# Kernel optimization log

Hardware: AMD Instinct MI355X
Metric: run time of the kernel (lower is better)

## Reference

```python
import jax, jax.numpy as jnp
import numpy as np
import math

DN = ('NCHW', 'OIHW', 'NCHW')

def conv(x, w, b, stride=1, pad=0):
    y = jax.lax.conv_general_dilated(x, w, (stride, stride), ((pad, pad), (pad, pad)), dimension_numbers=DN)
    return y + b[None, :, None, None]

def conv_t(x, w, b, stride=2, k=4, p=1):
    # torch ConvTranspose2d: weight (Cin, Cout, kH, kW). Equivalent fractionally-strided conv:
    w2 = jnp.transpose(w[:, :, ::-1, ::-1], (1, 0, 2, 3))  # -> (Cout, Cin, kH, kW), spatially flipped
    pp = k - 1 - p
    y = jax.lax.conv_general_dilated(x, w2, (1, 1), ((pp, pp), (pp, pp)), lhs_dilation=(stride, stride), dimension_numbers=DN)
    return y + b[None, :, None, None]

def res_stack(h, w1, b1, w2, b2):
    # w1: [L, rh, nh, 3, 3], w2: [L, nh, rh, 1, 1]
    for i in range(w1.shape[0]):
        t = conv(jax.nn.relu(h), w1[i], b1[i], 1, 1)
        t = conv(jax.nn.relu(t), w2[i], b2[i], 1, 0)
        h = h + t
    return jax.nn.relu(h)

def setup_inputs() -> dict:
    key = jax.random.key(0)
    ks = jax.random.split(key, 16)
    D, K = 64, 512
    limit = math.sqrt(3.0 / D)
    def w(k, shape, scale=0.05):
        return (jax.random.normal(k, shape, dtype=jnp.float32) * scale)
    return {
        'x': jax.random.normal(ks[0], (16, 3, 256, 256), dtype=jnp.float32),
        'enc_w0': w(ks[1], (64, 3, 4, 4)), 'enc_b0': jnp.zeros((64,), jnp.float32),
        'enc_w1': w(ks[2], (128, 64, 4, 4)), 'enc_b1': jnp.zeros((128,), jnp.float32),
        'enc_wf': w(ks[3], (128, 128, 3, 3)), 'enc_bf': jnp.zeros((128,), jnp.float32),
        'enc_res_w1': w(ks[4], (2, 32, 128, 3, 3)), 'enc_res_b1': jnp.zeros((2, 32), jnp.float32),
        'enc_res_w2': w(ks[5], (2, 128, 32, 1, 1)), 'enc_res_b2': jnp.zeros((2, 128), jnp.float32),
        'pre_w': w(ks[6], (64, 128, 1, 1)), 'pre_b': jnp.zeros((64,), jnp.float32),
        'codebook': jax.random.uniform(ks[7], (D, K), jnp.float32, -limit, limit),
        'dec_w': w(ks[8], (128, 64, 3, 3)), 'dec_b': jnp.zeros((128,), jnp.float32),
        'dec_res_w1': w(ks[9], (2, 32, 128, 3, 3)), 'dec_res_b1': jnp.zeros((2, 32), jnp.float32),
        'dec_res_w2': w(ks[10], (2, 128, 32, 1, 1)), 'dec_res_b2': jnp.zeros((2, 128), jnp.float32),
        'up_w0': w(ks[11], (128, 64, 4, 4)), 'up_b0': jnp.zeros((64,), jnp.float32),
        'up_w1': w(ks[12], (64, 3, 4, 4)), 'up_b1': jnp.zeros((3,), jnp.float32),
    }

def reference(x, enc_w0, enc_b0, enc_w1, enc_b1, enc_wf, enc_bf,
              enc_res_w1, enc_res_b1, enc_res_w2, enc_res_b2,
              pre_w, pre_b, codebook,
              dec_w, dec_b, dec_res_w1, dec_res_b1, dec_res_w2, dec_res_b2,
              up_w0, up_b0, up_w1, up_b1):
    # --- Encoder ---
    h = jax.nn.relu(conv(x, enc_w0, enc_b0, 2, 1))
    h = jax.nn.relu(conv(h, enc_w1, enc_b1, 2, 1))
    h = conv(h, enc_wf, enc_bf, 1, 1)
    h = res_stack(h, enc_res_w1, enc_res_b1, enc_res_w2, enc_res_b2)
    z = conv(h, pre_w, pre_b, 1, 0)  # [B, 64, 64, 64]
    # --- Vector quantizer (cdist + argmin + gather, straight-through) ---
    B, D, H, W = z.shape
    flat = jnp.transpose(z, (0, 2, 3, 1)).reshape(-1, D)  # [BHW, D]
    dist = (flat ** 2).sum(1, keepdims=True) - 2.0 * (flat @ codebook) + (codebook ** 2).sum(0)[None, :]
    idx = jnp.argmin(dist, axis=1)  # [BHW]
    q = codebook.T[idx].reshape(B, H, W, D).transpose(0, 3, 1, 2)
    zq = z + jax.lax.stop_gradient(q - z)  # straight-through estimator
    # --- Decoder ---
    h = conv(zq, dec_w, dec_b, 1, 1)
    h = res_stack(h, dec_res_w1, dec_res_b1, dec_res_w2, dec_res_b2)
    h = jax.nn.relu(conv_t(h, up_w0, up_b0, 2, 4, 1))
    x_recon = conv_t(h, up_w1, up_b1, 2, 4, 1)
    return x_recon
```

## Files before the change

### kernel.cpp

```cpp
#include <hip/hip_runtime.h>
#include <math.h>


#define DEV __device__ __forceinline__

DEV int rfl(int v) { return __builtin_amdgcn_readfirstlane(v); }

DEV void async_copy16(const float* g, float* l) {
  __builtin_amdgcn_global_load_lds(
      (const __attribute__((address_space(1))) void*)g,
      (__attribute__((address_space(3))) void*)l, 16, 0, 0);
}

typedef __attribute__((ext_vector_type(8))) _Float16 h16x8;
typedef __attribute__((ext_vector_type(4))) float f32x4;

DEV ushort f2h(float f) {
  _Float16 h = (_Float16)f;
  return __builtin_bit_cast(ushort, h);
}
DEV float h2f(ushort u) { return (float)__builtin_bit_cast(_Float16, u); }
DEV uint pk(ushort a, ushort b) { return (uint)a | ((uint)b << 16); }

template<int CIN, int COT>
__global__ __launch_bounds__(256) void prep_w3s(
    const float* __restrict__ w, ushort* __restrict__ wpk) {
  constexpr int nCh = CIN / 32, nM = COT / 16;
  const int t = blockIdx.x * 256 + threadIdx.x;
  if (t >= 9 * nCh * nM * 64) return;
  const int l = t & 63;
  const int m = (t >> 6) % nM;
  const int sid = t / (64 * nM);
  const int ch = sid / 9, khkw = sid % 9;
  const int co = m * 16 + (l & 15);
  const int k8 = (l >> 4) * 8;
  const int sw = (16 * l) ^ ((l & 4) ? 8 : 0);
  ushort* slab = wpk + (size_t)sid * (nM * 1024) + m * 1024;
#pragma unroll
  for (int i = 0; i < 8; i++) {
    const int ci = ch * 32 + k8 + i;
    const float v = w[((size_t)co * CIN + ci) * 9 + khkw];
    const ushort hi = f2h(v);
    slab[sw + i]       = hi;
    slab[(sw ^ 8) + i] = f2h((v - h2f(hi)) * 2048.0f);
  }
}

template<int CIN, int COT>
__global__ __launch_bounds__(256) void prep_w4s(
    const float* __restrict__ w, ushort* __restrict__ wpk) {
  const int t = blockIdx.x * 256 + threadIdx.x;
  if (t >= 16384) return;
  const int l = t & 63;
  const int m = (t >> 6) & 7;
  const int sid = t >> 9;
  const int step = sid >> 3, rr = (sid >> 2) & 1, kw = sid & 3;
  const int ch = step >> 1, h = step & 1;
  const int kh = 2 * h + rr;
  const int tap = kh * 4 + kw;
  const int co = m * 16 + (l & 15);
  const int k8 = (l >> 4) * 8;
  const int sw = (16 * l) ^ ((l & 4) ? 8 : 0);
  ushort* slab = wpk + (size_t)sid * 8192 + m * 1024;
#pragma unroll
  for (int i = 0; i < 8; i++) {
    const int ci = ch * 32 + k8 + i;
    const float v = w[((size_t)co * CIN + ci) * 16 + tap];
    const ushort hi = f2h(v);
    slab[sw + i]       = hi;
    slab[(sw ^ 8) + i] = f2h((v - h2f(hi)) * 2048.0f);
  }
}

template<int CIN, int COT>
__global__ __launch_bounds__(256) void prep_wts(
    const float* __restrict__ w, ushort* __restrict__ wpk) {
  constexpr int nCh = CIN / 32, nM = COT / 16;
  const int t = blockIdx.x * 256 + threadIdx.x;
  if (t >= 16 * nCh * nM * 64) return;
  const int l = t & 63;
  const int m = (t >> 6) % nM;
  const int sid = t / (64 * nM);
  const int ch = sid >> 4, idx = sid & 15;
  const int ord[16] = {15, 13, 14, 12, 7, 11, 5, 6, 9, 10, 4, 8, 3, 1, 2, 0};
  const int tap = ord[idx];
  const int kh = tap >> 2, kw = tap & 3;
  const int co = m * 16 + (l & 15);
  const int k8 = (l >> 4) * 8;
  const int sw = (16 * l) ^ ((l & 4) ? 8 : 0);
  ushort* slab = wpk + (size_t)sid * (nM * 1024) + m * 1024;
#pragma unroll
  for (int i = 0; i < 8; i++) {
    const int ci = ch * 32 + k8 + i;
    const float v = w[(((size_t)ci * COT + co) * 4 + kh) * 4 + kw];
    const ushort hi = f2h(v);
    slab[sw + i]       = hi;
    slab[(sw ^ 8) + i] = f2h((v - h2f(hi)) * 2048.0f);
  }
}

__global__ __launch_bounds__(256) void prep_cb(
    const float* __restrict__ cb, ushort* __restrict__ cbpk) {
  const int t = blockIdx.x * 256 + threadIdx.x;
  const int l = t & 63;
  const int m = (t >> 6) & 31;
  const int c = t >> 11;
  const int entry = m * 16 + (l & 15);
  ushort* o = cbpk + (size_t)t * 16;
#pragma unroll
  for (int i = 0; i < 8; i++) {
    const int d = c * 32 + (l >> 4) * 8 + i;
    const float v = cb[d * 512 + entry];
    const ushort hi = f2h(v);
    o[i]     = hi;
    o[8 + i] = f2h((v - h2f(hi)) * 2048.0f);
  }
}

__global__ __launch_bounds__(256) void cvt_cbn(
    const float* __restrict__ cb, float* __restrict__ cbn) {
  const int k = blockIdx.x * 256 + threadIdx.x;
  if (k >= 512) return;
  double s = 0.0;
  for (int d = 0; d < 64; d++) {
    const double c = (double)cb[d * 512 + k];
    s = fma(c, c, s);
  }
  cbn[k] = (float)s;
}

__global__ __launch_bounds__(256) void vq_mfma(
    const float* __restrict__ cb, const ushort* __restrict__ cbpk,
    const float* __restrict__ cbn, float* __restrict__ zq) {
  const int tid = threadIdx.x;
  const int l = tid & 63;
  const int w = rfl(tid >> 6);
  const int n = blockIdx.x >> 6, row = blockIdx.x & 63;
  float* zp = zq + (size_t)n * 262144 + row * 64;
  const int pos = w * 16 + (l & 15);

  h16x8 zh[2], zl[2];
#pragma unroll
  for (int c = 0; c < 2; c++) {
#pragma unroll
    for (int i = 0; i < 8; i++) {
      const int d = c * 32 + (l >> 4) * 8 + i;
      const float v = zp[(size_t)d * 4096 + pos];
      const _Float16 h = (_Float16)v;
      zh[c][i] = h;
      zl[c][i] = (_Float16)((v - (float)h) * 2048.0f);
    }
  }

  const float SCL = 1.0f / 2048.0f;
  float bestd = 1e30f;
  int best = 0;
  for (int grp = 0; grp < 4; grp++) {
    f32x4 aH[8], aM[8];
#pragma unroll
    for (int m = 0; m < 8; m++) {
      aH[m] = (f32x4){0.f, 0.f, 0.f, 0.f};
      aM[m] = (f32x4){0.f, 0.f, 0.f, 0.f};
    }
#pragma unroll
    for (int c = 0; c < 2; c++) {
#pragma unroll
      for (int m = 0; m < 8; m++) {
        const ushort* ap = cbpk + ((size_t)(c * 32 + grp * 8 + m) * 64 + l) * 16;
        const h16x8 ah = *(const h16x8*)ap;
        const h16x8 al = *(const h16x8*)(ap + 8);
        aH[m] = __builtin_amdgcn_mfma_f32_16x16x32_f16(ah, zh[c], aH[m], 0, 0, 0);
        aM[m] = __builtin_amdgcn_mfma_f32_16x16x32_f16(al, zh[c], aM[m], 0, 0, 0);
        aM[m] = __builtin_amdgcn_mfma_f32_16x16x32_f16(ah, zl[c], aM[m], 0, 0, 0);
      }
    }
#pragma unroll
    for (int m = 0; m < 8; m++) {
#pragma unroll
      for (int j = 0; j < 4; j++) {
        const int k = grp * 128 + m * 16 + ((l >> 4) << 2) + j;
        const float dd = aH[m][j] + aM[m][j] * SCL;
        const float dist = fmaf(-2.0f, dd, cbn[k]);
        if (dist < bestd) { bestd = dist; best = k; }
      }
    }
  }

#pragma unroll
  for (int off = 16; off <= 32; off <<= 1) {
    const float d2 = __shfl_xor(bestd, off, 64);
    const int i2 = __shfl_xor(best, off, 64);
    if (d2 < bestd || (d2 == bestd && i2 < best)) { bestd = d2; best = i2; }
  }

#pragma unroll
  for (int i = 0; i < 16; i++) {
    const int d = (l >> 4) * 16 + i;
    zp[(size_t)d * 4096 + pos] = cb[d * 512 + best];
  }
}

template<int CIN, int COT, bool RELU_OUT>
__global__ __launch_bounds__(256, 2) void conv4s2_mfma(
    const float* __restrict__ x, const ushort* __restrict__ wpk,
    const float* __restrict__ bias, float* __restrict__ y) {
  constexpr int nCh = CIN / 32, nM = COT / 16;
  constexpr int nStep = nCh * 2;
  constexpr int nTap = nStep * 8;
  __shared__ ushort act[2][2][2][66][40];
  __shared__ ushort wlds[2][8192];
  const int tid = threadIdx.x;
  const int l = tid & 63;
  const int wv = rfl(tid >> 6);
  const int ho = (blockIdx.x & 7) * 8 + (blockIdx.x >> 3);
  const int n = blockIdx.z;

  {
    uint* lp = (uint*)&act[0][0][0][0][0];
    for (int s = tid; s < 16 * 20; s += 256) {
      const int c = s / 20, w32 = s % 20;
      const int which = c & 1, rest = c >> 1;
      lp[(size_t)(rest * 66 + (which ? 65 : 0)) * 20 + w32] = 0;
    }
  }

  const float* xn = x + ((size_t)n * CIN) * 16384;

  float2 sreg[2][4][2];
  float rmask[2];
  auto LOADG = [&](int step) {
    const int ch = step >> 1, h = step & 1;
#pragma unroll
    for (int rr = 0; rr < 2; rr++) {
      const int ir = 2 * ho - 1 + 2 * h + rr;
      const bool ok = (ir >= 0) && (ir < 128);
      const int irc = ok ? ir : 0;
      rmask[rr] = ok ? 1.0f : 0.0f;
#pragma unroll
      for (int cc = 0; cc < 4; cc++) {
        const int ci0 = ch * 32 + cc * 8 + wv * 2;
        sreg[rr][cc][0] = *(const float2*)(xn + (size_t)ci0 * 16384 + irc * 128 + 2 * l);
        sreg[rr][cc][1] = *(const float2*)(xn + (size_t)(ci0 + 1) * 16384 + irc * 128 + 2 * l);
      }
    }
  };
  auto WRITE = [&]() {
    uint* base = (uint*)&act[0][0][0][0][0];
#pragma unroll
    for (int rr = 0; rr < 2; rr++) {
#pragma unroll
      for (int cc = 0; cc < 4; cc++) {
        const float e0 = sreg[rr][cc][0].x * rmask[rr], o0 = sreg[rr][cc][0].y * rmask[rr];
        const float e1 = sreg[rr][cc][1].x * rmask[rr], o1 = sreg[rr][cc][1].y * rmask[rr];
        const ushort he0 = f2h(e0), ho_0 = f2h(o0);
        const ushort he1 = f2h(e1), ho_1 = f2h(o1);
        const ushort le0 = f2h((e0 - h2f(he0)) * 2048.0f);
        const ushort lo0 = f2h((o0 - h2f(ho_0)) * 2048.0f);
        const ushort le1 = f2h((e1 - h2f(he1)) * 2048.0f);
        const ushort lo1 = f2h((o1 - h2f(ho_1)) * 2048.0f);
        const int u = cc * 4 + wv;
        const size_t sl20 = (size_t)(l + 1) * 20 + u;
        base[(size_t)((0 * 2 + rr) * 2 + 0) * 1320 + sl20] = pk(he0, he1);
        base[(size_t)((0 * 2 + rr) * 2 + 1) * 1320 + sl20] = pk(ho_0, ho_1);
        base[(size_t)((1 * 2 + rr) * 2 + 0) * 1320 + sl20] = pk(le0, le1);
        base[(size_t)((1 * 2 + rr) * 2 + 1) * 1320 + sl20] = pk(lo0, lo1);
      }
    }
  };
  auto STAGEW = [&](int t, int buf) {
    const ushort* src = wpk + (size_t)t * 8192;
    ushort* dst = &wlds[buf][0];
#pragma unroll
    for (int j = 0; j < 4; j++)
      async_copy16((const float*)(src + (j * 256 + tid) * 8),
                   (float*)(dst + (j * 256 + tid) * 8));
  };

  f32x4 accH[nM], accM[nM];
#pragma unroll
  for (int m = 0; m < nM; m++) {
    const int co = m * 16 + ((l >> 4) << 2);
    accH[m] = (f32x4){bias[co], bias[co + 1], bias[co + 2], bias[co + 3]};
    accM[m] = (f32x4){0.f, 0.f, 0.f, 0.f};
  }

  const int pb = wv * 16;
  const int sw = (16 * l) ^ ((l & 4) ? 8 : 0);
  STAGEW(0, 0);
  LOADG(0);
  int tcnt = 0;
  for (int step = 0; step < nStep; step++) {
    __syncthreads();
    WRITE();
    __syncthreads();
#pragma unroll
    for (int rr = 0; rr < 2; rr++) {
#pragma unroll
      for (int kw = 0; kw < 4; kw++) {
        if (!(rr == 0 && kw == 0)) __syncthreads();
        if (tcnt + 1 < nTap) STAGEW(tcnt + 1, (tcnt + 1) & 1);
        if (rr == 0 && kw == 0 && step + 1 < nStep) LOADG(step + 1);
        const ushort* wb = &wlds[tcnt & 1][0];
        const int eo = (kw == 0 || kw == 2) ? 1 : 0;
        const int sh = (kw == 0) ? 0 : (kw == 3) ? 2 : 1;
        const int sl = pb + (l & 15) + sh;
        const h16x8 bh = *(const h16x8*)(&act[0][rr][eo][sl][(l >> 4) * 8]);
        const h16x8 bl = *(const h16x8*)(&act[1][rr][eo][sl][(l >> 4) * 8]);
#pragma unroll
        for (int m = 0; m < nM; m++) {
          const h16x8 ah = *(const h16x8*)(wb + m * 1024 + sw);
          const h16x8 al = *(const h16x8*)(wb + m * 1024 + (sw ^ 8));
          accH[m] = __builtin_amdgcn_mfma_f32_16x16x32_f16(ah, bh, accH[m], 0, 0, 0);
          accM[m] = __builtin_amdgcn_mfma_f32_16x16x32_f16(al, bh, accM[m], 0, 0, 0);
          accM[m] = __builtin_amdgcn_mfma_f32_16x16x32_f16(ah, bl, accM[m], 0, 0, 0);
        }
        tcnt++;
      }
    }
  }

  const float SCL = 1.0f / 2048.0f;
  const int pos = pb + (l & 15);
  const int r4 = (l >> 4) << 2;
#pragma unroll
  for (int m = 0; m < nM; m++) {
    const int co = m * 16 + r4;
    float* yp = y + (((size_t)(n * COT + co)) * 64 + ho) * 64 + pos;
#pragma unroll
    for (int j = 0; j < 4; j++) {
      float v = accH[m][j] + accM[m][j] * SCL;
      if (RELU_OUT) v = fmaxf(v, 0.f);
      yp[(size_t)j * 4096] = v;
    }
  }
}

template<int CIN, int COT, int TILE, bool RELU_IN>
__global__ __launch_bounds__(256, 2) void conv3_mfma2(
    const float* __restrict__ x, const ushort* __restrict__ wpk,
    const float* __restrict__ bias, float* __restrict__ y) {
  constexpr int nCh = CIN / 32, nMf = COT / 16, nMt = TILE / 16;
  constexpr int nTap = nCh * 9;
  __shared__ ushort act[2][4 * 66 * 40];
  __shared__ ushort wlds[2][nMt * 1024];
  const int tid = threadIdx.x;
  const int l = tid & 63;
  const int wv = rfl(tid >> 6);
  const int r0 = blockIdx.x * 2;
  const int hblk = blockIdx.y;
  const int n = blockIdx.z;

  {
    uint* lp = (uint*)&act[0][0];
    for (int s = tid; s < 16 * 20; s += 256) {
      const int c = s / 20, w32 = s % 20;
      const int which = c & 1;
      const int rowrel = (c >> 1) & 3;
      const int plane  = c >> 3;
      lp[(size_t)(plane * 264 + rowrel * 66 + (which ? 65 : 0)) * 20 + w32] = 0;
    }
  }

  const float* xn = x + ((size_t)n * CIN) * 4096;

  float sreg[4][4][2];
  auto LOADG = [&](int ch) {
#pragma unroll
    for (int rr = 0; rr < 4; rr++) {
      const int ir = r0 - 1 + rr;
      const bool ok = (ir >= 0) && (ir < 64);
#pragma unroll
      for (int cc = 0; cc < 4; cc++) {
        const int ci0 = ch * 32 + cc * 8 + wv * 2;
        sreg[rr][cc][0] = ok ? xn[((size_t)ci0 * 64 + ir) * 64 + l] : 0.f;
        sreg[rr][cc][1] = ok ? xn[((size_t)(ci0 + 1) * 64 + ir) * 64 + l] : 0.f;
      }
    }
  };
  auto WRITE = [&]() {
    uint* ph = (uint*)&act[0][0];
    uint* pl = (uint*)&act[1][0];
#pragma unroll
    for (int rr = 0; rr < 4; rr++) {
#pragma unroll
      for (int cc = 0; cc < 4; cc++) {
        float v0 = sreg[rr][cc][0], v1 = sreg[rr][cc][1];
        if (RELU_IN) { v0 = fmaxf(v0, 0.f); v1 = fmaxf(v1, 0.f); }
        const ushort h0 = f2h(v0), h1 = f2h(v1);
        const ushort m0 = f2h((v0 - h2f(h0)) * 2048.0f);
        const ushort m1 = f2h((v1 - h2f(h1)) * 2048.0f);
        const int idx = (rr * 66 + (l + 1)) * 20 + cc * 4 + wv;
        ph[idx] = (uint)h0 | ((uint)h1 << 16);
        pl[idx] = (uint)m0 | ((uint)m1 << 16);
      }
    }
  };
  auto STAGEW = [&](int t, int buf) {
    const ushort* src = wpk + (size_t)t * (nMf * 1024) + hblk * (nMt * 1024);
    ushort* dst = &wlds[buf][0];
#pragma unroll
    for (int j = 0; j < nMt / 2; j++)
      async_copy16((const float*)(src + (j * 256 + tid) * 8),
                   (float*)(dst + (j * 256 + tid) * 8));
  };

  f32x4 accH[2][nMt], accM[2][nMt];
#pragma unroll
  for (int m = 0; m < nMt; m++) {
    const int co = hblk * TILE + m * 16 + ((l >> 4) << 2);
    const f32x4 b4 = (f32x4){bias[co], bias[co + 1], bias[co + 2], bias[co + 3]};
#pragma unroll
    for (int ro = 0; ro < 2; ro++) {
      accH[ro][m] = b4;
      accM[ro][m] = (f32x4){0.f, 0.f, 0.f, 0.f};
    }
  }

  const int pb = wv * 16;
  const int sw = (16 * l) ^ ((l & 4) ? 8 : 0);
  STAGEW(0, 0);
  LOADG(0);
  int tcnt = 0;
  for (int ch = 0; ch < nCh; ch++) {
    __syncthreads();
    WRITE();
    __syncthreads();
#pragma unroll
    for (int kh = 0; kh < 3; kh++) {
#pragma unroll
      for (int kw = 0; kw < 3; kw++) {
        if (!(kh == 0 && kw == 0)) __syncthreads();
        if (tcnt + 1 < nTap) STAGEW(tcnt + 1, (tcnt + 1) & 1);
        if (kh == 0 && kw == 0 && ch + 1 < nCh) LOADG(ch + 1);
        const ushort* wb = &wlds[tcnt & 1][0];
        h16x8 bh[2], bl[2];
#pragma unroll
        for (int ro = 0; ro < 2; ro++) {
          const int slot = (ro + kh) * 66 + pb + (l & 15) + kw;
          bh[ro] = *(const h16x8*)(&act[0][0] + slot * 40 + (l >> 4) * 8);
          bl[ro] = *(const h16x8*)(&act[1][0] + slot * 40 + (l >> 4) * 8);
        }
#pragma unroll
        for (int m = 0; m < nMt; m++) {
          const h16x8 ah = *(const h16x8*)(wb + m * 1024 + sw);
          const h16x8 al = *(const h16x8*)(wb + m * 1024 + (sw ^ 8));
#pragma unroll
          for (int ro = 0; ro < 2; ro++) {
            accH[ro][m] = __builtin_amdgcn_mfma_f32_16x16x32_f16(ah, bh[ro], accH[ro][m], 0, 0, 0);
            accM[ro][m] = __builtin_amdgcn_mfma_f32_16x16x32_f16(al, bh[ro], accM[ro][m], 0, 0, 0);
            accM[ro][m] = __builtin_amdgcn_mfma_f32_16x16x32_f16(ah, bl[ro], accM[ro][m], 0, 0, 0);
          }
        }
        tcnt++;
      }
    }
  }

  const float SCL = 1.0f / 2048.0f;
  const int pos = pb + (l & 15);
  const int r4 = (l >> 4) << 2;
#pragma unroll
  for (int ro = 0; ro < 2; ro++) {
#pragma unroll
    for (int m = 0; m < nMt; m++) {
      const int co = hblk * TILE + m * 16 + r4;
      float* yp = y + (((size_t)(n * COT + co)) * 64 + (r0 + ro)) * 64 + pos;
#pragma unroll
      for (int j = 0; j < 4; j++)
        yp[(size_t)j * 4096] = accH[ro][m][j] + accM[ro][m][j] * SCL;
    }
  }
}

template<int CIN, int COT, bool RELU_OUT>
__global__ __launch_bounds__(256, 2) void convt_mfma(
    const float* __restrict__ x, const ushort* __restrict__ wpk,
    const float* __restrict__ bias, float* __restrict__ y) {
  constexpr int nCh = CIN / 32, nM = COT / 16;
  constexpr int nPair = nCh * 8;
  __shared__ ushort act[2][3 * 66 * 40];
  __shared__ ushort wlds[2][2 * nM * 1024];
  const int tid = threadIdx.x;
  const int l = tid & 63;
  const int wv = rfl(tid >> 6);
  const int a = blockIdx.x;
  const int n = blockIdx.z;

  {
    uint* lp = (uint*)&act[0][0];
    for (int s = tid; s < 12 * 20; s += 256) {
      const int c = s / 20, w32 = s % 20;
      const int which = c & 1;
      const int rowrel = (c >> 1) % 3;
      const int plane  = (c >> 1) / 3;
      lp[(size_t)(plane * 198 + rowrel * 66 + (which ? 65 : 0)) * 20 + w32] = 0;
    }
  }

  const float* xn = x + ((size_t)n * CIN) * 4096;

  float sreg[3][4][2];
  auto LOADG = [&](int ch) {
#pragma unroll
    for (int rr = 0; rr < 3; rr++) {
      const int ir = a - 1 + rr;
      const bool ok = (ir >= 0) && (ir < 64);
#pragma unroll
      for (int cc = 0; cc < 4; cc++) {
        const int ci0 = ch * 32 + cc * 8 + wv * 2;
        sreg[rr][cc][0] = ok ? xn[((size_t)ci0 * 64 + ir) * 64 + l] : 0.f;
        sreg[rr][cc][1] = ok ? xn[((size_t)(ci0 + 1) * 64 + ir) * 64 + l] : 0.f;
      }
    }
  };
  auto WRITE = [&]() {
    uint* ph = (uint*)&act[0][0];
    uint* pl = (uint*)&act[1][0];
#pragma unroll
    for (int rr = 0; rr < 3; rr++) {
#pragma unroll
      for (int cc = 0; cc < 4; cc++) {
        const float v0 = sreg[rr][cc][0], v1 = sreg[rr][cc][1];
        const ushort h0 = f2h(v0), h1 = f2h(v1);
        const ushort m0 = f2h((v0 - h2f(h0)) * 2048.0f);
        const ushort m1 = f2h((v1 - h2f(h1)) * 2048.0f);
        const int idx = (rr * 66 + (l + 1)) * 20 + cc * 4 + wv;
        ph[idx] = (uint)h0 | ((uint)h1 << 16);
        pl[idx] = (uint)m0 | ((uint)m1 << 16);
      }
    }
  };
  auto STAGEW2 = [&](int p, int buf) {
    const ushort* src = wpk + (size_t)p * (2 * nM * 1024);
    ushort* dst = &wlds[buf][0];
#pragma unroll
    for (int j = 0; j < nM; j++)
      async_copy16((const float*)(src + (j * 256 + tid) * 8),
                   (float*)(dst + (j * 256 + tid) * 8));
  };

  f32x4 aH[4][nM], aM[4][nM];
#pragma unroll
  for (int m = 0; m < nM; m++) {
    const int co = m * 16 + ((l >> 4) << 2);
    const f32x4 b4 = (f32x4){bias[co], bias[co + 1], bias[co + 2], bias[co + 3]};
#pragma unroll
    for (int o = 0; o < 4; o++) { aH[o][m] = b4; aM[o][m] = (f32x4){0.f,0.f,0.f,0.f}; }
  }

  const int pb = wv * 16;
  const int sw = (16 * l) ^ ((l & 4) ? 8 : 0);
  STAGEW2(0, 0);
  LOADG(0);
  int pcnt = 0;

#define CT_TAP(WOFS, RR, DD, OIDX) {                                          \
    const int slot = (RR) * 66 + pb + (l & 15) + 1 + (DD);                    \
    const h16x8 bh = *(const h16x8*)(&act[0][0] + slot * 40 + (l >> 4) * 8);  \
    const h16x8 bl = *(const h16x8*)(&act[1][0] + slot * 40 + (l >> 4) * 8);  \
    _Pragma("unroll")                                                         \
    for (int m = 0; m < nM; m++) {                                            \
      const h16x8 ah = *(const h16x8*)(wb + (WOFS) + m * 1024 + sw);          \
      const h16x8 al = *(const h16x8*)(wb + (WOFS) + m * 1024 + (sw ^ 8));    \
      aH[OIDX][m] = __builtin_amdgcn_mfma_f32_16x16x32_f16(ah, bh, aH[OIDX][m], 0, 0, 0); \
      aM[OIDX][m] = __builtin_amdgcn_mfma_f32_16x16x32_f16(al, bh, aM[OIDX][m], 0, 0, 0); \
      aM[OIDX][m] = __builtin_amdgcn_mfma_f32_16x16x32_f16(ah, bl, aM[OIDX][m], 0, 0, 0); \
    }}
#define CT_PHASE(RRA, DDA, OA, RRB, DDB, OB) {                                \
    if (!first) __syncthreads();                                              \
    first = false;                                                            \
    if (pcnt + 1 < nPair) STAGEW2(pcnt + 1, (pcnt + 1) & 1);                  \
    if (doLoad) { if (ch + 1 < nCh) LOADG(ch + 1); doLoad = false; }          \
    const ushort* wb = &wlds[pcnt & 1][0];                                    \
    CT_TAP(0, RRA, DDA, OA)                                                   \
    CT_TAP(nM * 1024, RRB, DDB, OB)                                           \
    pcnt++; }

  for (int ch = 0; ch < nCh; ch++) {
    __syncthreads();
    WRITE();
    __syncthreads();
    bool first = true, doLoad = true;
    CT_PHASE(0, -1, 0,  0,  0, 0)
    CT_PHASE(0,  0, 1,  0, +1, 1)
    CT_PHASE(1, -1, 0,  1, -1, 2)
    CT_PHASE(1,  0, 0,  1,  0, 1)
    CT_PHASE(1,  0, 2,  1,  0, 3)
    CT_PHASE(1, +1, 1,  1, +1, 3)
    CT_PHASE(2, -1, 2,  2,  0, 2)
    CT_PHASE(2,  0, 3,  2, +1, 3)
  }
#undef CT_TAP
#undef CT_PHASE

  const float SCL = 1.0f / 2048.0f;
  const int b = pb + (l & 15);
  const int oh0 = 2 * a;
  const int r4 = (l >> 4) << 2;
#pragma unroll
  for (int m = 0; m < nM; m++) {
    const int co = m * 16 + r4;
#pragma unroll
    for (int j = 0; j < 4; j++) {
      float v0e = aH[0][m][j] + aM[0][m][j] * SCL;
      float v0o = aH[1][m][j] + aM[1][m][j] * SCL;
      float v1e = aH[2][m][j] + aM[2][m][j] * SCL;
      float v1o = aH[3][m][j] + aM[3][m][j] * SCL;
      if (RELU_OUT) {
        v0e = fmaxf(v0e, 0.f); v0o = fmaxf(v0o, 0.f);
        v1e = fmaxf(v1e, 0.f); v1o = fmaxf(v1o, 0.f);
      }
      float* row0 = y + (((size_t)(n * COT + co + j)) * 128 + oh0) * 128;
      ((float2*)row0)[b] = make_float2(v0e, v0o);
      ((float2*)(row0 + 128))[b] = make_float2(v1e, v1o);
    }
  }
}

template<int CIN, int COT, bool RELU_OUT, int OW>
__global__ __launch_bounds__(256) void conv4s2_row(
    const float* __restrict__ x, const float* __restrict__ w,
    const float* __restrict__ bias, float* __restrict__ y,
    int Hout, int Cout) {
  const int Win = OW * 2, Hin = Hout * 2;
  const int t = blockIdx.x * 256 + threadIdx.x;
  const int wo = t & (OW - 1);
  const int ho = rfl(t / OW);
  const int co0 = blockIdx.y * COT, n = blockIdx.z;

  float acc[COT];
#pragma unroll
  for (int u = 0; u < COT; u++) acc[u] = bias[co0 + u];

  const int iw0 = 2 * wo - 1;
  const int cA = iw0 < 0 ? 0 : iw0;
  const bool mA = iw0 >= 0;
  const int cD = (iw0 + 3 < Win) ? iw0 + 3 : Win - 1;
  const bool mD = iw0 + 3 < Win;

  for (int ci = 0; ci < CIN; ci++) {
    const float* xp = x + ((size_t)(n * CIN + ci)) * Hin * Win;
    const float* wp = w + ((size_t)(co0 * CIN + ci)) * 16;
#pragma unroll
    for (int kh = 0; kh < 4; kh++) {
      const int ih = 2 * ho - 1 + kh;
      if (ih >= 0 && ih < Hin) {
        const float* row = xp + (size_t)ih * Win;
        float x0 = row[cA];      x0 = mA ? x0 : 0.f;
        float x1 = row[iw0 + 1];
        float x2 = row[iw0 + 2];
        float x3 = row[cD];      x3 = mD ? x3 : 0.f;
#pragma unroll
        for (int u = 0; u < COT; u++) {
          const float* wr = wp + u * CIN * 16 + kh * 4;
          acc[u] = fmaf(x0, wr[0], acc[u]);
          acc[u] = fmaf(x1, wr[1], acc[u]);
          acc[u] = fmaf(x2, wr[2], acc[u]);
          acc[u] = fmaf(x3, wr[3], acc[u]);
        }
      }
    }
  }
#pragma unroll
  for (int u = 0; u < COT; u++) {
    float v = acc[u];
    if (RELU_OUT) v = fmaxf(v, 0.f);
    y[(((size_t)(n * Cout + co0 + u)) * Hout + ho) * OW + wo] = v;
  }
}

template<int CIN, int COT, bool RELU_IN, bool ACCUM, bool RELU_OUT>
__global__ __launch_bounds__(256) void conv1x1_v4(
    const float* __restrict__ x, const float* __restrict__ w,
    const float* __restrict__ bias, float* __restrict__ y,
    int HW, int Cout) {
  const int p = (blockIdx.x * 256 + threadIdx.x) * 4;
  const int co0 = blockIdx.y * COT, n = blockIdx.z;

  float4 acc[COT];
#pragma unroll
  for (int u = 0; u < COT; u++) {
    const float b = bias[co0 + u];
    acc[u] = make_float4(b, b, b, b);
  }
  for (int ci = 0; ci < CIN; ci++) {
    float4 xv = *(const float4*)&x[((size_t)(n * CIN + ci)) * HW + p];
    if (RELU_IN) {
      xv.x = fmaxf(xv.x, 0.f); xv.y = fmaxf(xv.y, 0.f);
      xv.z = fmaxf(xv.z, 0.f); xv.w = fmaxf(xv.w, 0.f);
    }
#pragma unroll
    for (int u = 0; u < COT; u++) {
      const float wv = w[(co0 + u) * CIN + ci];
      acc[u].x = fmaf(xv.x, wv, acc[u].x);
      acc[u].y = fmaf(xv.y, wv, acc[u].y);
      acc[u].z = fmaf(xv.z, wv, acc[u].z);
      acc[u].w = fmaf(xv.w, wv, acc[u].w);
    }
  }
#pragma unroll
  for (int u = 0; u < COT; u++) {
    float4* yp = (float4*)&y[((size_t)(n * Cout + co0 + u)) * HW + p];
    float4 r = acc[u];
    if (ACCUM) {
      float4 h = *yp;
      r.x += h.x; r.y += h.y; r.z += h.z; r.w += h.w;
    }
    if (RELU_OUT) {
      r.x = fmaxf(r.x, 0.f); r.y = fmaxf(r.y, 0.f);
      r.z = fmaxf(r.z, 0.f); r.w = fmaxf(r.w, 0.f);
    }
    *yp = r;
  }
}

template<int CIN, int COT, bool RELU_IN, bool RELU_OUT, int WH>
__global__ __launch_bounds__(256) void convt_row(
    const float* __restrict__ x, const float* __restrict__ w,
    const float* __restrict__ bias, float* __restrict__ y,
    int Hin, int Cout) {
  const int Hout = Hin * 2;
  const int t = blockIdx.x * 256 + threadIdx.x;
  const int a = t & (WH - 1);
  const int oh = rfl(t / WH);
  const int co0 = blockIdx.y * COT, n = blockIdx.z;

  float acc0[COT], acc1[COT];
#pragma unroll
  for (int u = 0; u < COT; u++) { acc0[u] = bias[co0 + u]; acc1[u] = bias[co0 + u]; }

  const int cm = a > 0 ? a - 1 : 0;
  const bool mm = a > 0;
  const int cp = a < WH - 1 ? a + 1 : WH - 1;
  const bool mp = a < WH - 1;

  const int kh0 = (oh + 1) & 1;
#pragma unroll
  for (int dh = 0; dh < 2; dh++) {
    const int kh = kh0 + 2 * dh;
    const int ih = (oh + 1 - kh) >> 1;
    if (ih >= 0 && ih < Hin) {
      for (int ci = 0; ci < CIN; ci++) {
        const float* row = x + (((size_t)(n * CIN + ci)) * Hin + ih) * WH;
        float x0  = row[a];
        float xm1 = row[cm];  xm1 = mm ? xm1 : 0.f;
        float xp1 = row[cp];  xp1 = mp ? xp1 : 0.f;
        if (RELU_IN) {
          x0 = fmaxf(x0, 0.f); xm1 = fmaxf(xm1, 0.f); xp1 = fmaxf(xp1, 0.f);
        }
        const float* wp = w + ((size_t)(ci * Cout + co0)) * 16 + kh * 4;
#pragma unroll
        for (int u = 0; u < COT; u++) {
          const float* wr = wp + u * 16;
          acc0[u] = fmaf(x0,  wr[1], acc0[u]);
          acc0[u] = fmaf(xm1, wr[3], acc0[u]);
          acc1[u] = fmaf(xp1, wr[0], acc1[u]);
          acc1[u] = fmaf(x0,  wr[2], acc1[u]);
        }
      }
    }
  }
#pragma unroll
  for (int u = 0; u < COT; u++) {
    float v0 = acc0[u], v1 = acc1[u];
    if (RELU_OUT) { v0 = fmaxf(v0, 0.f); v1 = fmaxf(v1, 0.f); }
    float* row = y + (((size_t)(n * Cout + co0 + u)) * Hout + oh) * (2 * WH);
    ((float2*)row)[a] = make_float2(v0, v1);
  }
}

extern "C" void kernel_launch(void* const* d_in, const int* in_sizes, int n_in,
                              void* d_out, int out_size, void* d_ws, size_t ws_size,
                              hipStream_t stream) {
  const float* x          = (const float*)d_in[0];
  const float* enc_w0     = (const float*)d_in[1];
  const float* enc_b0     = (const float*)d_in[2];
  const float* enc_w1     = (const float*)d_in[3];
  const float* enc_b1     = (const float*)d_in[4];
  const float* enc_wf     = (const float*)d_in[5];
  const float* enc_bf     = (const float*)d_in[6];
  const float* enc_res_w1 = (const float*)d_in[7];
  const float* enc_res_b1 = (const float*)d_in[8];
  const float* enc_res_w2 = (const float*)d_in[9];
  const float* enc_res_b2 = (const float*)d_in[10];
  const float* pre_w      = (const float*)d_in[11];
  const float* pre_b      = (const float*)d_in[12];
  const float* codebook   = (const float*)d_in[13];
  const float* dec_w      = (const float*)d_in[14];
  const float* dec_b      = (const float*)d_in[15];
  const float* dec_res_w1 = (const float*)d_in[16];
  const float* dec_res_b1 = (const float*)d_in[17];
  const float* dec_res_w2 = (const float*)d_in[18];
  const float* dec_res_b2 = (const float*)d_in[19];
  const float* up_w0      = (const float*)d_in[20];
  const float* up_b0      = (const float*)d_in[21];
  const float* up_w1      = (const float*)d_in[22];
  const float* up_b1      = (const float*)d_in[23];
  float* out = (float*)d_out;

  float* A = (float*)d_ws;
  float* B = A + 16777216;
  float* C = B + 8388608;
  ushort* wpkF  = (ushort*)(A + 8388608);
  ushort* wpkEa = wpkF  + 294912;
  ushort* wpkEb = wpkEa + 73728;
  ushort* wpkD  = wpkEb + 73728;
  ushort* wpkDa = wpkD  + 147456;
  ushort* wpkDb = wpkDa + 73728;
  ushort* cbpk  = wpkDb + 73728;
  float*  cbn   = (float*)(cbpk + 131072);
  ushort* wpk1  = (ushort*)C;
  ushort* wpkT  = wpk1 + 262144;

  const dim3 blk(256);
  const int N = 16;

  prep_w4s<64, 128><<<dim3(64), blk, 0, stream>>>(enc_w1, wpk1);

  conv4s2_row<3, 16, true, 128><<<dim3(64, 4, N), blk, 0, stream>>>(
      x, enc_w0, enc_b0, A, 128, 64);
  conv4s2_mfma<64, 128, true><<<dim3(64, 1, N), blk, 0, stream>>>(
      A, wpk1, enc_b1, B);

  prep_w3s<128, 128><<<dim3(72), blk, 0, stream>>>(enc_wf, wpkF);
  prep_w3s<128, 32><<<dim3(18), blk, 0, stream>>>(enc_res_w1, wpkEa);
  prep_w3s<128, 32><<<dim3(18), blk, 0, stream>>>(
      enc_res_w1 + (size_t)32 * 128 * 9, wpkEb);
  prep_w3s<64, 128><<<dim3(36), blk, 0, stream>>>(dec_w, wpkD);
  prep_w3s<128, 32><<<dim3(18), blk, 0, stream>>>(dec_res_w1, wpkDa);
  prep_w3s<128, 32><<<dim3(18), blk, 0, stream>>>(
      dec_res_w1 + (size_t)32 * 128 * 9, wpkDb);
  prep_cb<<<dim3(16), blk, 0, stream>>>(codebook, cbpk);
  cvt_cbn<<<dim3(2), blk, 0, stream>>>(codebook, cbn);

  conv3_mfma2<128, 128, 64, false><<<dim3(32, 2, N), blk, 0, stream>>>(
      B, wpkF, enc_bf, C);
  conv3_mfma2<128, 32, 32, true><<<dim3(32, 1, N), blk, 0, stream>>>(
      C, wpkEa, enc_res_b1, A);
  conv1x1_v4<32, 8, true, true, false><<<dim3(4, 16, N), blk, 0, stream>>>(
      A, enc_res_w2, enc_res_b2, C, 4096, 128);
  conv3_mfma2<128, 32, 32, true><<<dim3(32, 1, N), blk, 0, stream>>>(
      C, wpkEb, enc_res_b1 + 32, A);
  conv1x1_v4<32, 8, true, true, true><<<dim3(4, 16, N), blk, 0, stream>>>(
      A, enc_res_w2 + (size_t)128 * 32, enc_res_b2 + 128, C, 4096, 128);
  conv1x1_v4<128, 8, false, false, false><<<dim3(4, 8, N), blk, 0, stream>>>(
      C, pre_w, pre_b, A, 4096, 64);

  prep_wts<128, 64><<<dim3(64), blk, 0, stream>>>(up_w0, wpkT);

  vq_mfma<<<dim3(1024), blk, 0, stream>>>(codebook, cbpk, cbn, A);

  conv3_mfma2<64, 128, 64, false><<<dim3(32, 2, N), blk, 0, stream>>>(
      A, wpkD, dec_b, B);
  conv3_mfma2<128, 32, 32, true><<<dim3(32, 1, N), blk, 0, stream>>>(
      B, wpkDa, dec_res_b1, A);
  conv1x1_v4<32, 8, true, true, false><<<dim3(4, 16, N), blk, 0, stream>>>(
      A, dec_res_w2, dec_res_b2, B, 4096, 128);
  conv3_mfma2<128, 32, 32, true><<<dim3(32, 1, N), blk, 0, stream>>>(
      B, wpkDb, dec_res_b1 + 32, A);
  conv1x1_v4<32, 8, true, true, true><<<dim3(4, 16, N), blk, 0, stream>>>(
      A, dec_res_w2 + (size_t)128 * 32, dec_res_b2 + 128, B, 4096, 128);
  convt_mfma<128, 64, true><<<dim3(64, 1, N), blk, 0, stream>>>(
      B, wpkT, up_b0, A);
  convt_row<64, 3, false, false, 128><<<dim3(128, 1, N), blk, 0, stream>>>(
      A, up_w1, up_b1, out, 128, 3);
}
```

Before: 725.5 us.

## Move 1x1 convolutions onto MFMA with split-fp16 packed weights

Replaces the scalar FMA conv1x1 kernel with an MFMA kernel that uses hi/lo fp16 splitting of both weights and activations, keeping accuracy close to fp32. A new prep kernel packs the 1x1 weights into the MFMA operand layout. Each block now computes all output channels for 64 pixels, so the input is read once per block rather than once per group of 8 output channels. The cost is extra prep launches and three MFMAs per tile, and the per-lane activation loads are strided by HW with only 16 contiguous pixels per row.

```diff
diff --git a/kernel.cpp b/kernel.cpp
--- a/kernel.cpp
+++ b/kernel.cpp
@@ -99,6 +99,28 @@
   }
 }
 
+template<int CIN, int COT>
+__global__ __launch_bounds__(256) void prep_w1(
+    const float* __restrict__ w, ushort* __restrict__ wpk) {
+  constexpr int nCh = CIN / 32, nM = COT / 16;
+  const int t = blockIdx.x * 256 + threadIdx.x;
+  if (t >= nCh * nM * 64) return;
+  const int l = t & 63;
+  const int m = (t >> 6) % nM;
+  const int kc = t / (64 * nM);
+  const int co = m * 16 + (l & 15);
+  const int k8 = (l >> 4) * 8;
+  ushort* o = wpk + (size_t)t * 16;
+#pragma unroll
+  for (int i = 0; i < 8; i++) {
+    const int ci = kc * 32 + k8 + i;
+    const float v = w[(size_t)co * CIN + ci];
+    const ushort hi = f2h(v);
+    o[i]     = hi;
+    o[8 + i] = f2h((v - h2f(hi)) * 2048.0f);
+  }
+}
+
 __global__ __launch_bounds__(256) void prep_cb(
     const float* __restrict__ cb, ushort* __restrict__ cbpk) {
   const int t = blockIdx.x * 256 + threadIdx.x;
@@ -197,6 +219,65 @@
   for (int i = 0; i < 16; i++) {
     const int d = (l >> 4) * 16 + i;
     zp[(size_t)d * 4096 + pos] = cb[d * 512 + best];
+  }
+}
+
+template<int CIN, int COT, bool RELU_IN, bool ACCUM, bool RELU_OUT>
+__global__ __launch_bounds__(256) void conv1x1_mfma(
+    const float* __restrict__ x, const ushort* __restrict__ wpk,
+    const float* __restrict__ bias, float* __restrict__ y, int HW) {
+  constexpr int nCh = CIN / 32, nM = COT / 16;
+  const int tid = threadIdx.x;
+  const int l = tid & 63;
+  const int wv = rfl(tid >> 6);
+  const int n = blockIdx.z;
+  const int p = blockIdx.x * 64 + wv * 16 + (l & 15);
+
+  const float* xp = x + (size_t)n * CIN * HW + p;
+
+  f32x4 accH[nM], accM[nM];
+#pragma unroll
+  for (int m = 0; m < nM; m++) {
+    const int co = m * 16 + ((l >> 4) << 2);
+    accH[m] = (f32x4){bias[co], bias[co + 1], bias[co + 2], bias[co + 3]};
+    accM[m] = (f32x4){0.f, 0.f, 0.f, 0.f};
+  }
+
+#pragma unroll
+  for (int kc = 0; kc < nCh; kc++) {
+    h16x8 zh, zl;
+#pragma unroll
+    for (int i = 0; i < 8; i++) {
+      const int ci = kc * 32 + (l >> 4) * 8 + i;
+      float v = xp[(size_t)ci * HW];
+      if (RELU_IN) v = fmaxf(v, 0.f);
+      const _Float16 h = (_Float16)v;
+      zh[i] = h;
+      zl[i] = (_Float16)((v - (float)h) * 2048.0f);
+    }
+#pragma unroll
+    for (int m = 0; m < nM; m++) {
+      const ushort* ap = wpk + ((size_t)(kc * nM + m) * 64 + l) * 16;
+      const h16x8 ah = *(const h16x8*)ap;
+      const h16x8 al = *(const h16x8*)(ap + 8);
+      accH[m] = __builtin_amdgcn_mfma_f32_16x16x32_f16(ah, zh, accH[m], 0, 0, 0);
+      accM[m] = __builtin_amdgcn_mfma_f32_16x16x32_f16(al, zh, accM[m], 0, 0, 0);
+      accM[m] = __builtin_amdgcn_mfma_f32_16x16x32_f16(ah, zl, accM[m], 0, 0, 0);
+    }
+  }
+
+  const float SCL = 1.0f / 2048.0f;
+#pragma unroll
+  for (int m = 0; m < nM; m++) {
+    const int co = m * 16 + ((l >> 4) << 2);
+    float* yp = y + ((size_t)n * COT + co) * HW + p;
+#pragma unroll
+    for (int j = 0; j < 4; j++) {
+      float r = accH[m][j] + accM[m][j] * SCL;
+      if (ACCUM) r += yp[(size_t)j * HW];
+      if (RELU_OUT) r = fmaxf(r, 0.f);
+      yp[(size_t)j * HW] = r;
+    }
   }
 }
 
@@ -666,51 +747,6 @@
     float v = acc[u];
     if (RELU_OUT) v = fmaxf(v, 0.f);
     y[(((size_t)(n * Cout + co0 + u)) * Hout + ho) * OW + wo] = v;
-  }
-}
-
-template<int CIN, int COT, bool RELU_IN, bool ACCUM, bool RELU_OUT>
-__global__ __launch_bounds__(256) void conv1x1_v4(
-    const float* __restrict__ x, const float* __restrict__ w,
-    const float* __restrict__ bias, float* __restrict__ y,
-    int HW, int Cout) {
-  const int p = (blockIdx.x * 256 + threadIdx.x) * 4;
-  const int co0 = blockIdx.y * COT, n = blockIdx.z;
-
-  float4 acc[COT];
-#pragma unroll
-  for (int u = 0; u < COT; u++) {
-    const float b = bias[co0 + u];
-    acc[u] = make_float4(b, b, b, b);
-  }
-  for (int ci = 0; ci < CIN; ci++) {
-    float4 xv = *(const float4*)&x[((size_t)(n * CIN + ci)) * HW + p];
-    if (RELU_IN) {
-      xv.x = fmaxf(xv.x, 0.f); xv.y = fmaxf(xv.y, 0.f);
-      xv.z = fmaxf(xv.z, 0.f); xv.w = fmaxf(xv.w, 0.f);
-    }
-#pragma unroll
-    for (int u = 0; u < COT; u++) {
-      const float wv = w[(co0 + u) * CIN + ci];
-      acc[u].x = fmaf(xv.x, wv, acc[u].x);
-      acc[u].y = fmaf(xv.y, wv, acc[u].y);
-      acc[u].z = fmaf(xv.z, wv, acc[u].z);
-      acc[u].w = fmaf(xv.w, wv, acc[u].w);
-    }
-  }
-#pragma unroll
-  for (int u = 0; u < COT; u++) {
-    float4* yp = (float4*)&y[((size_t)(n * Cout + co0 + u)) * HW + p];
-    float4 r = acc[u];
-    if (ACCUM) {
-      float4 h = *yp;
-      r.x += h.x; r.y += h.y; r.z += h.z; r.w += h.w;
-    }
-    if (RELU_OUT) {
-      r.x = fmaxf(r.x, 0.f); r.y = fmaxf(r.y, 0.f);
-      r.z = fmaxf(r.z, 0.f); r.w = fmaxf(r.w, 0.f);
-    }
-    *yp = r;
   }
 }
 
@@ -809,6 +845,11 @@
   ushort* wpkDb = wpkDa + 73728;
   ushort* cbpk  = wpkDb + 73728;
   float*  cbn   = (float*)(cbpk + 131072);
+  ushort* wpkR2Ea = cbpk + 131072 + 1024;
+  ushort* wpkR2Eb = wpkR2Ea + 8192;
+  ushort* wpkR2Da = wpkR2Eb + 8192;
+  ushort* wpkR2Db = wpkR2Da + 8192;
+  ushort* wpkP    = wpkR2Db + 8192;
   ushort* wpk1  = (ushort*)C;
   ushort* wpkT  = wpk1 + 262144;
 
@@ -832,19 +873,26 @@
       dec_res_w1 + (size_t)32 * 128 * 9, wpkDb);
   prep_cb<<<dim3(16), blk, 0, stream>>>(codebook, cbpk);
   cvt_cbn<<<dim3(2), blk, 0, stream>>>(codebook, cbn);
+  prep_w1<32, 128><<<dim3(2), blk, 0, stream>>>(enc_res_w2, wpkR2Ea);
+  prep_w1<32, 128><<<dim3(2), blk, 0, stream>>>(
+      enc_res_w2 + (size_t)128 * 32, wpkR2Eb);
+  prep_w1<32, 128><<<dim3(2), blk, 0, stream>>>(dec_res_w2, wpkR2Da);
+  prep_w1<32, 128><<<dim3(2), blk, 0, stream>>>(
+      dec_res_w2 + (size_t)128 * 32, wpkR2Db);
+  prep_w1<128, 64><<<dim3(4), blk, 0, stream>>>(pre_w, wpkP);
 
   conv3_mfma2<128, 128, 64, false><<<dim3(32, 2, N), blk, 0, stream>>>(
       B, wpkF, enc_bf, C);
   conv3_mfma2<128, 32, 32, true><<<dim3(32, 1, N), blk, 0, stream>>>(
       C, wpkEa, enc_res_b1, A);
-  conv1x1_v4<32, 8, true, true, false><<<dim3(4, 16, N), blk, 0, stream>>>(
-      A, enc_res_w2, enc_res_b2, C, 4096, 128);
+  conv1x1_mfma<32, 128, true, true, false><<<dim3(64, 1, N), blk, 0, stream>>>(
+      A, wpkR2Ea, enc_res_b2, C, 4096);
   conv3_mfma2<128, 32, 32, true><<<dim3(32, 1, N), blk, 0, stream>>>(
       C, wpkEb, enc_res_b1 + 32, A);
-  conv1x1_v4<32, 8, true, true, true><<<dim3(4, 16, N), blk, 0, stream>>>(
-      A, enc_res_w2 + (size_t)128 * 32, enc_res_b2 + 128, C, 4096, 128);
-  conv1x1_v4<128, 8, false, false, false><<<dim3(4, 8, N), blk, 0, stream>>>(
-      C, pre_w, pre_b, A, 4096, 64);
+  conv1x1_mfma<32, 128, true, true, true><<<dim3(64, 1, N), blk, 0, stream>>>(
+      A, wpkR2Eb, enc_res_b2 + 128, C, 4096);
+  conv1x1_mfma<128, 64, false, false, false><<<dim3(64, 1, N), blk, 0, stream>>>(
+      C, wpkP, pre_b, A, 4096);
 
   prep_wts<128, 64><<<dim3(64), blk, 0, stream>>>(up_w0, wpkT);
 
@@ -854,12 +902,12 @@
       A, wpkD, dec_b, B);
   conv3_mfma2<128, 32, 32, true><<<dim3(32, 1, N), blk, 0, stream>>>(
       B, wpkDa, dec_res_b1, A);
-  conv1x1_v4<32, 8, true, true, false><<<dim3(4, 16, N), blk, 0, stream>>>(
-      A, dec_res_w2, dec_res_b2, B, 4096, 128);
+  conv1x1_mfma<32, 128, true, true, false><<<dim3(64, 1, N), blk, 0, stream>>>(
+      A, wpkR2Da, dec_res_b2, B, 4096);
   conv3_mfma2<128, 32, 32, true><<<dim3(32, 1, N), blk, 0, stream>>>(
       B, wpkDb, dec_res_b1 + 32, A);
-  conv1x1_v4<32, 8, true, true, true><<<dim3(4, 16, N), blk, 0, stream>>>(
-      A, dec_res_w2 + (size_t)128 * 32, dec_res_b2 + 128, B, 4096, 128);
+  conv1x1_mfma<32, 128, true, true, true><<<dim3(64, 1, N), blk, 0, stream>>>(
+      A, wpkR2Db, dec_res_b2 + 128, B, 4096);
   convt_mfma<128, 64, true><<<dim3(64, 1, N), blk, 0, stream>>>(
       B, wpkT, up_b0, A);
   convt_row<64, 3, false, false, 128><<<dim3(128, 1, N), blk, 0, stream>>>(
```

After: 697.4 us. -3.9%, faster.
